# Performance work log

Measured on AMD Instinct MI355X. Metric: run time of the kernel, lower is better.

The kernel has to match this reference:

```python
import jax, jax.numpy as jnp
import numpy as np

B = 16384
DIM = 1024
HEADS = 16
LN_EPS = 1e-5


def setup_inputs() -> dict:
    key = jax.random.key(0)
    ks = jax.random.split(key, 8)
    d = DIM
    s = 0.02
    return {
        "x_u": jax.random.normal(ks[0], (B, d), dtype=jnp.float32),
        "x_m": jax.random.normal(ks[1], (B, d), dtype=jnp.float32),
        # MHA m2u (path 1): packed in_proj [3d, d] like torch, out_proj [d, d]
        "w_qkv1": (jax.random.normal(ks[2], (3 * d, d), dtype=jnp.float32) * s),
        "b_qkv1": jnp.zeros((3 * d,), dtype=jnp.float32),
        "w_o1": (jax.random.normal(ks[3], (d, d), dtype=jnp.float32) * s),
        "b_o1": jnp.zeros((d,), dtype=jnp.float32),
        # MHA u2m (path 2)
        "w_qkv2": (jax.random.normal(ks[4], (3 * d, d), dtype=jnp.float32) * s),
        "b_qkv2": jnp.zeros((3 * d,), dtype=jnp.float32),
        "w_o2": (jax.random.normal(ks[5], (d, d), dtype=jnp.float32) * s),
        "b_o2": jnp.zeros((d,), dtype=jnp.float32),
        # proj head: LayerNorm(2d) + Linear(2d -> d) + GELU (dropout = eval identity)
        "ln_g": jnp.ones((2 * d,), dtype=jnp.float32),
        "ln_b": jnp.zeros((2 * d,), dtype=jnp.float32),
        "w_proj": (jax.random.normal(ks[6], (d, 2 * d), dtype=jnp.float32) * s),
        "b_proj": jnp.zeros((d,), dtype=jnp.float32),
        "heads": HEADS,
    }


def _mha_single_token(xq, xkv, w_qkv, b_qkv, w_o, b_o, heads):
    # seq_len = 1 cross-attention: softmax over a single key is exactly 1.
    d = xq.shape[-1]
    dh = d // heads
    wq, wk, wv = jnp.split(w_qkv, 3, axis=0)
    bq, bk, bv = jnp.split(b_qkv, 3)
    q = (xq @ wq.T + bq).reshape(-1, heads, dh)   # [B, H, dh]
    k = (xkv @ wk.T + bk).reshape(-1, heads, dh)
    v = (xkv @ wv.T + bv).reshape(-1, heads, dh)
    scores = jnp.sum(q * k, axis=-1) / jnp.sqrt(jnp.asarray(dh, q.dtype))  # [B, H]
    attn = jax.nn.softmax(scores[..., None], axis=-1)  # singleton key axis -> ones
    out = (attn * v).reshape(-1, d)                    # [B, d]
    return out @ w_o.T + b_o


def reference(x_u, x_m, w_qkv1, b_qkv1, w_o1, b_o1,
              w_qkv2, b_qkv2, w_o2, b_o2,
              ln_g, ln_b, w_proj, b_proj, heads):
    # Path 1: Q = x_m, K/V = x_u ; Path 2: Q = x_u, K/V = x_m
    z1 = _mha_single_token(x_m, x_u, w_qkv1, b_qkv1, w_o1, b_o1, heads)
    z2 = _mha_single_token(x_u, x_m, w_qkv2, b_qkv2, w_o2, b_o2, heads)
    z = jnp.concatenate([z1, z2], axis=-1)  # [B, 2d]
    mu = jnp.mean(z, axis=-1, keepdims=True)
    var = jnp.mean(jnp.square(z - mu), axis=-1, keepdims=True)
    zn = (z - mu) * jax.lax.rsqrt(var + LN_EPS) * ln_g + ln_b
    h = zn @ w_proj.T + b_proj               # [B, d]
    return jax.nn.gelu(h, approximate=False)  # torch nn.GELU default = exact erf
```

## Files before the change

### kernel.cpp

```cpp
#include <hip/hip_runtime.h>
#include <cstdint>


#define DIM 1024
#define BROWS 16384

typedef __bf16 bf16x8 __attribute__((ext_vector_type(8)));
typedef float f32x4 __attribute__((ext_vector_type(4)));

__device__ __forceinline__ ushort f2bf(float f) {
    uint32_t u = __builtin_bit_cast(uint32_t, f);
    u = (u + 0x7fffu + ((u >> 16) & 1u)) >> 16;
    return (ushort)u;
}

__device__ __forceinline__ void async_copy16(const void* gsrc, void* ldst) {
    __builtin_amdgcn_global_load_lds(
        (__attribute__((address_space(1))) void*)((uintptr_t)gsrc),
        (__attribute__((address_space(3))) void*)((uint32_t)(uintptr_t)ldst),
        16, 0, 0);
}

__global__ __launch_bounds__(256) void prep_kernel(
        const float* __restrict__ x_u, const float* __restrict__ x_m,
        const float* __restrict__ wqkv1, const float* __restrict__ bqkv1,
        const float* __restrict__ wo1, const float* __restrict__ bo1,
        const float* __restrict__ wqkv2, const float* __restrict__ bqkv2,
        const float* __restrict__ wo2, const float* __restrict__ bo2,
        const float* __restrict__ lng, const float* __restrict__ lnb,
        const float* __restrict__ wproj, const float* __restrict__ bproj,
        ushort* __restrict__ x_bf, ushort* __restrict__ wo12,
        ushort* __restrict__ wvT12, ushort* __restrict__ Wp,
        float* __restrict__ b12, float* __restrict__ Svec, float* __restrict__ Cvec,
        float* __restrict__ sums) {
    const int b = blockIdx.x, t = threadIdx.x;
    __shared__ float red[4][4];
    __shared__ float tls[32][33];

    if (b < 8192) {
        const int n4 = (BROWS * DIM) / 4;
        int i = b * 256 + t;
        const int stride = 8192 * 256;
        const float4* xu4 = (const float4*)x_u;
        const float4* xm4 = (const float4*)x_m;
        ushort4* o4 = (ushort4*)x_bf;
#pragma unroll
        for (int it = 0; it < 4; it++, i += stride) {
            float4 v = (i < n4) ? xu4[i] : xm4[i - n4];
            ushort4 o;
            o.x = f2bf(v.x); o.y = f2bf(v.y); o.z = f2bf(v.z); o.w = f2bf(v.w);
            o4[i] = o;
        }
    } else if (b < 9216) {
        int j = b - 8192;
        float s1 = 0.f, s2 = 0.f, sS = 0.f, sC = 0.f;
        for (int c = t; c < DIM; c += 256) {
            s1 += wo1[j * DIM + c] * bqkv1[2 * DIM + c];
            s2 += wo2[j * DIM + c] * bqkv2[2 * DIM + c];
        }
        for (int c = t; c < 2 * DIM; c += 256) {
            float w = wproj[j * 2 * DIM + c];
            sS += w * lng[c];
            sC += w * lnb[c];
        }
        for (int o = 32; o; o >>= 1) {
            s1 += __shfl_down(s1, o, 64);
            s2 += __shfl_down(s2, o, 64);
            sS += __shfl_down(sS, o, 64);
            sC += __shfl_down(sC, o, 64);
        }
        int wid = t >> 6;
        if ((t & 63) == 0) { red[wid][0] = s1; red[wid][1] = s2; red[wid][2] = sS; red[wid][3] = sC; }
        __syncthreads();
        if (t == 0) {
            s1 = red[0][0] + red[1][0] + red[2][0] + red[3][0];
            s2 = red[0][1] + red[1][1] + red[2][1] + red[3][1];
            sS = red[0][2] + red[1][2] + red[2][2] + red[3][2];
            sC = red[0][3] + red[1][3] + red[2][3] + red[3][3];
            b12[j]       = s1 + bo1[j];
            b12[DIM + j] = s2 + bo2[j];
            Svec[j] = sS;
            Cvec[j] = sC + bproj[j];
        }
    } else if (b < 12288) {
        const int NWO = (DIM * DIM) / 4;
        const int NWP = (DIM * 2 * DIM) / 4;
        const int total = 2 * NWO + NWP;
        int i = (b - 9216) * 256 + t;
        const int stride = 3072 * 256;
        for (; i < total; i += stride) {
            if (i < 2 * NWO) {
                float4 v = (i < NWO) ? ((const float4*)wo1)[i] : ((const float4*)wo2)[i - NWO];
                ushort4 o;
                o.x = f2bf(v.x); o.y = f2bf(v.y); o.z = f2bf(v.z); o.w = f2bf(v.w);
                ((ushort4*)wo12)[i] = o;
            } else {
                int j = i - 2 * NWO;
                float4 v = ((const float4*)wproj)[j];
                int c = (j * 4) & (2 * DIM - 1);
                v.x *= lng[c]; v.y *= lng[c + 1]; v.z *= lng[c + 2]; v.w *= lng[c + 3];
                ushort4 o;
                o.x = f2bf(v.x); o.y = f2bf(v.y); o.z = f2bf(v.z); o.w = f2bf(v.w);
                ((ushort4*)Wp)[j] = o;
            }
        }
    } else if (b < 14336) {
        int tile = b - 12288;
        int z = tile >> 10;
        int t2 = tile & 1023;
        int mt = t2 >> 5, kt = t2 & 31;
        const float* src = z ? wqkv2 : wqkv1;
        int tr = t >> 3;
        int tc4 = (t & 7) * 4;
        const float* p = src + (long)(2 * DIM + mt * 32 + tr) * DIM + kt * 32 + tc4;
        float4 v = *(const float4*)p;
        tls[tr][tc4 + 0] = v.x; tls[tr][tc4 + 1] = v.y;
        tls[tr][tc4 + 2] = v.z; tls[tr][tc4 + 3] = v.w;
        __syncthreads();
        ushort4 o;
        o.x = f2bf(tls[tc4 + 0][tr]);
        o.y = f2bf(tls[tc4 + 1][tr]);
        o.z = f2bf(tls[tc4 + 2][tr]);
        o.w = f2bf(tls[tc4 + 3][tr]);
        *(ushort4*)(wvT12 + (long)z * DIM * DIM + (long)(kt * 32 + tr) * DIM + mt * 32 + tc4) = o;
    } else {
        int i = (b - 14336) * 256 + t;
        ((float4*)sums)[i] = float4{0.f, 0.f, 0.f, 0.f};
    }
}

__global__ __launch_bounds__(256, 2) void gemm_w(
        const ushort* __restrict__ Ag, const ushort* __restrict__ Wg,
        ushort* __restrict__ Cg, int K, int lda, int ldw, int ldc,
        long sAz, long sWz, long sCz) {
    constexpr int BM = 64, BN = 64, BK = 32;
    constexpr int MT = BM / 32;
    constexpr int NT = BN / 32;
    __shared__ __align__(16) ushort As[BM * BK];
    __shared__ __align__(16) ushort Bs[BN * BK];
    const int tid = threadIdx.x;
    const int wid = tid >> 6;
    const int lane = tid & 63;
    const int quad = lane >> 4;
    const int l16 = lane & 15;
    const int waveM = wid >> 1, waveN = wid & 1;
    const int zb = blockIdx.z;

    const ushort* A = Ag + zb * sAz + (long)blockIdx.x * BM * lda;
    const ushort* W = Wg + zb * sWz + (long)blockIdx.y * BN * ldw;

    f32x4 acc[MT][NT] = {};
    constexpr int nA = (BM * BK) / (256 * 8);
    constexpr int nB = (BN * BK) / (256 * 8);
    const int swz = (l16 >> 1) & 3;
    const int rdA = quad ^ swz;
    for (int k0 = 0; k0 < K; k0 += BK) {
#pragma unroll
        for (int c = 0; c < nA; c++) {
            int idx = c * 256 + tid;
            int r = idx >> 2;
            int q = (idx & 3) ^ ((r >> 1) & 3);
            async_copy16(A + (long)r * lda + k0 + q * 8, (char*)As + (c * 256 + wid * 64) * 16);
        }
#pragma unroll
        for (int c = 0; c < nB; c++) {
            int idx = c * 256 + tid;
            int r = idx >> 2;
            int q = (idx & 3) ^ ((r >> 1) & 3);
            async_copy16(W + (long)r * ldw + k0 + q * 8, (char*)Bs + (c * 256 + wid * 64) * 16);
        }
        asm volatile("s_waitcnt vmcnt(0)" ::: "memory");
        __syncthreads();

        bf16x8 af[MT], bfg[NT];
#pragma unroll
        for (int im = 0; im < MT; im++)
            af[im] = *(const bf16x8*)(As + (waveM * (BM / 2) + im * 16 + l16) * BK + rdA * 8);
#pragma unroll
        for (int in = 0; in < NT; in++)
            bfg[in] = *(const bf16x8*)(Bs + (waveN * (BN / 2) + in * 16 + l16) * BK + rdA * 8);
#pragma unroll
        for (int im = 0; im < MT; im++)
#pragma unroll
            for (int in = 0; in < NT; in++)
                acc[im][in] = __builtin_amdgcn_mfma_f32_16x16x32_bf16(
                    af[im], bfg[in], acc[im][in], 0, 0, 0);
        __syncthreads();
    }

    const int gRow0 = blockIdx.x * BM + waveM * (BM / 2) + quad * 4;
    const int gCol0 = blockIdx.y * BN + waveN * (BN / 2) + l16;
    ushort* C = Cg + zb * sCz;
#pragma unroll
    for (int im = 0; im < MT; im++)
#pragma unroll
        for (int in = 0; in < NT; in++) {
            int col = gCol0 + in * 16;
#pragma unroll
            for (int r = 0; r < 4; r++) {
                int row = gRow0 + im * 16 + r;
                C[(long)row * ldc + col] = f2bf(acc[im][in][r]);
            }
        }
}

template <int MODE>
__global__ __launch_bounds__(256, 2) void gemm_bt2(
        const ushort* __restrict__ Ag, const ushort* __restrict__ Wg,
        void* __restrict__ Cg, int K, int lda, int ldw, int ldc,
        long sAz, long sWz, long sCz,
        const float* __restrict__ bias,
        const float* __restrict__ Svec, const float* __restrict__ Cvec,
        float* __restrict__ sumbuf, float* __restrict__ sqbuf) {
    __shared__ __align__(16) ushort As[3 * 8192];
    __shared__ __align__(16) ushort Bs[3 * 4096];
    const int tid = threadIdx.x;
    const int wid = tid >> 6;
    const int lane = tid & 63;
    const int quad = lane >> 4;
    const int l16 = lane & 15;
    const int waveM = wid >> 1;
    const int waveN = wid & 1;
    const int zb = blockIdx.z;
    const int rd = quad ^ ((l16 >> 1) & 3);

    const ushort* A = Ag + zb * sAz + (long)blockIdx.x * 256 * lda;
    const ushort* W = Wg + zb * sWz + (long)blockIdx.y * 128 * ldw;
    const int NTK = K >> 5;

    f32x4 acc[8][4] = {};

#pragma unroll
    for (int u = 0; u < 2; ++u) {
        const int k0 = u << 5;
        char* sa = (char*)As + u * 16384;
        char* sb = (char*)Bs + u * 8192;
#pragma unroll
        for (int rnd = 0; rnd < 4; ++rnd) {
            int idx = rnd * 256 + tid;
            int r = idx >> 2;
            int q = (idx & 3) ^ ((r >> 1) & 3);
            async_copy16(A + (long)r * lda + k0 + q * 8, sa + (rnd * 256 + wid * 64) * 16);
        }
#pragma unroll
        for (int rnd = 0; rnd < 2; ++rnd) {
            int idx = rnd * 256 + tid;
            int r = idx >> 2;
            int q = (idx & 3) ^ ((r >> 1) & 3);
            async_copy16(W + (long)r * ldw + k0 + q * 8, sb + (rnd * 256 + wid * 64) * 16);
        }
    }
    asm volatile("s_waitcnt vmcnt(6)" ::: "memory");
    __builtin_amdgcn_s_barrier();
    asm volatile("" ::: "memory");

    int cs = 0, ss = 2;
    for (int t = 0; t < NTK; ++t) {
        const ushort* as = As + cs * 8192;
        const ushort* bs = Bs + cs * 4096;

        bf16x8 af[8], bfg[4];
#pragma unroll
        for (int j = 0; j < 4; ++j)
            bfg[j] = *(const bf16x8*)(bs + (waveN * 64 + j * 16 + l16) * 32 + rd * 8);
#pragma unroll
        for (int i = 0; i < 8; ++i)
            af[i] = *(const bf16x8*)(as + (waveM * 128 + i * 16 + l16) * 32 + rd * 8);

        const int u = t + 2;
        if (u < NTK) {
            const int k0u = u << 5;
            char* sa = (char*)As + ss * 16384;
            char* sb = (char*)Bs + ss * 8192;
#pragma unroll
            for (int rnd = 0; rnd < 4; ++rnd) {
                int idx = rnd * 256 + tid;
                int r = idx >> 2;
                int q = (idx & 3) ^ ((r >> 1) & 3);
                async_copy16(A + (long)r * lda + k0u + q * 8, sa + (rnd * 256 + wid * 64) * 16);
            }
#pragma unroll
            for (int rnd = 0; rnd < 2; ++rnd) {
                int idx = rnd * 256 + tid;
                int r = idx >> 2;
                int q = (idx & 3) ^ ((r >> 1) & 3);
                async_copy16(W + (long)r * ldw + k0u + q * 8, sb + (rnd * 256 + wid * 64) * 16);
            }
        }

        __builtin_amdgcn_s_setprio(1);
#pragma unroll
        for (int i = 0; i < 8; ++i)
#pragma unroll
            for (int j = 0; j < 4; ++j)
                acc[i][j] = __builtin_amdgcn_mfma_f32_16x16x32_bf16(
                    af[i], bfg[j], acc[i][j], 0, 0, 0);
        __builtin_amdgcn_s_setprio(0);

        if (t < NTK - 1) {
            if (t < NTK - 2) asm volatile("s_waitcnt vmcnt(6)" ::: "memory");
            else             asm volatile("s_waitcnt vmcnt(0)" ::: "memory");
            __builtin_amdgcn_s_barrier();
            asm volatile("" ::: "memory");
        }
        cs = (cs == 2) ? 0 : cs + 1;
        ss = (ss == 2) ? 0 : ss + 1;
    }

    const int gRow0 = blockIdx.x * 256 + waveM * 128 + quad * 4;
    const int gCol0 = blockIdx.y * 128 + waveN * 64 + l16;
    if constexpr (MODE == 1) {
        ushort* C = (ushort*)Cg + zb * sCz;
#pragma unroll
        for (int im = 0; im < 8; ++im) {
            float sr[4] = {0.f, 0.f, 0.f, 0.f};
            float qr[4] = {0.f, 0.f, 0.f, 0.f};
#pragma unroll
            for (int in = 0; in < 4; ++in) {
                int col = gCol0 + in * 16;
                float badd = bias[zb * DIM + col];
#pragma unroll
                for (int r = 0; r < 4; ++r) {
                    int row = gRow0 + im * 16 + r;
                    float val = acc[im][in][r] + badd;
                    C[(long)row * ldc + col] = f2bf(val);
                    sr[r] += val;
                    qr[r] += val * val;
                }
            }
#pragma unroll
            for (int r = 0; r < 4; ++r) {
                float s = sr[r], q = qr[r];
#pragma unroll
                for (int o = 1; o < 16; o <<= 1) {
                    s += __shfl_xor(s, o, 64);
                    q += __shfl_xor(q, o, 64);
                }
                if (l16 == 0) {
                    int row = gRow0 + im * 16 + r;
                    atomicAdd(&sumbuf[row], s);
                    atomicAdd(&sqbuf[row], q);
                }
            }
        }
    } else {
        float* O = (float*)Cg;
#pragma unroll
        for (int im = 0; im < 8; ++im) {
#pragma unroll
            for (int r = 0; r < 4; ++r) {
                int row = gRow0 + im * 16 + r;
                float sv = sumbuf[row], qv = sqbuf[row];
                float m = sv * (1.f / 2048.f);
                float var = qv * (1.f / 2048.f) - m * m;
                float rstd = rsqrtf(var + 1e-5f);
#pragma unroll
                for (int in = 0; in < 4; ++in) {
                    int col = gCol0 + in * 16;
                    float h = rstd * (acc[im][in][r] - m * Svec[col]) + Cvec[col];
                    O[(long)row * ldc + col] = 0.5f * h * (1.0f + erff(h * 0.7071067811865475f));
                }
            }
        }
    }
}


extern "C" void kernel_launch(void* const* d_in, const int* in_sizes, int n_in,
                              void* d_out, int out_size, void* d_ws, size_t ws_size,
                              hipStream_t stream) {
    (void)in_sizes; (void)n_in; (void)out_size; (void)ws_size;
    const float* x_u   = (const float*)d_in[0];
    const float* x_m   = (const float*)d_in[1];
    const float* wqkv1 = (const float*)d_in[2];
    const float* bqkv1 = (const float*)d_in[3];
    const float* wo1   = (const float*)d_in[4];
    const float* bo1   = (const float*)d_in[5];
    const float* wqkv2 = (const float*)d_in[6];
    const float* bqkv2 = (const float*)d_in[7];
    const float* wo2   = (const float*)d_in[8];
    const float* bo2   = (const float*)d_in[9];
    const float* lng   = (const float*)d_in[10];
    const float* lnb   = (const float*)d_in[11];
    const float* wproj = (const float*)d_in[12];
    const float* bproj = (const float*)d_in[13];

    char* ws = (char*)d_ws;
    ushort* x_bf  = (ushort*)(ws + 0);
    ushort* wo12  = (ushort*)(ws + 67108864);
    ushort* wvT12 = (ushort*)(ws + 71303168);
    ushort* W12   = (ushort*)(ws + 75497472);
    ushort* Wp    = (ushort*)(ws + 79691776);
    ushort* zbuf  = (ushort*)(ws + 83886080);
    float*  b12   = (float*)(ws + 150994944);
    float*  Svec  = (float*)(ws + 151003136);
    float*  Cvec  = (float*)(ws + 151007232);
    float*  sumbuf= (float*)(ws + 151011328);
    float*  sqbuf = (float*)(ws + 151076864);

    prep_kernel<<<14368, 256, 0, stream>>>(
        x_u, x_m, wqkv1, bqkv1, wo1, bo1, wqkv2, bqkv2, wo2, bo2,
        lng, lnb, wproj, bproj,
        x_bf, wo12, wvT12, Wp, b12, Svec, Cvec, sumbuf);

    gemm_w<<<dim3(16, 16, 2), 256, 0, stream>>>(
        wo12, wvT12, W12, DIM, DIM, DIM, DIM,
        (long)DIM * DIM, (long)DIM * DIM, (long)DIM * DIM);

    gemm_bt2<1><<<dim3(64, 8, 2), 256, 0, stream>>>(
        x_bf, W12, zbuf, DIM, DIM, DIM, 2 * DIM,
        (long)BROWS * DIM, (long)DIM * DIM, (long)DIM,
        b12, nullptr, nullptr, sumbuf, sqbuf);

    gemm_bt2<2><<<dim3(64, 8, 1), 256, 0, stream>>>(
        zbuf, Wp, d_out, 2 * DIM, 2 * DIM, 2 * DIM, DIM,
        0, 0, 0,
        nullptr, Svec, Cvec, sumbuf, sqbuf);
}
```

Baseline: 402.9 us.

## Widen GEMM tiles to 256x256 with BK=64, 512 threads, double buffering

The two main bf16 GEMMs now use 512-thread blocks with 256x256 output tiles and a 64-wide K step. The old 256x128 tiles used a 32-wide K step with triple buffering. Shared-memory staging switches to an 8-way XOR swizzle with two sub-k MFMA passes per stage and a plain double buffer that waits for vmcnt(0) every iteration. The larger tile is meant to raise arithmetic intensity and halve the number of barriers per K. The cost is 128KB of LDS per block, which likely limits occupancy to one block per CU, and less prefetch depth, since each wait drains all loads.

```diff
diff --git a/kernel.cpp b/kernel.cpp
--- a/kernel.cpp
+++ b/kernel.cpp
@@ -205,110 +205,89 @@
 }
 
 template <int MODE>
-__global__ __launch_bounds__(256, 2) void gemm_bt2(
+__global__ __launch_bounds__(512, 2) void gemm_bk64(
         const ushort* __restrict__ Ag, const ushort* __restrict__ Wg,
         void* __restrict__ Cg, int K, int lda, int ldw, int ldc,
         long sAz, long sWz, long sCz,
         const float* __restrict__ bias,
         const float* __restrict__ Svec, const float* __restrict__ Cvec,
         float* __restrict__ sumbuf, float* __restrict__ sqbuf) {
-    __shared__ __align__(16) ushort As[3 * 8192];
-    __shared__ __align__(16) ushort Bs[3 * 4096];
+    __shared__ __align__(16) ushort As[2 * 16384];
+    __shared__ __align__(16) ushort Bs[2 * 16384];
     const int tid = threadIdx.x;
     const int wid = tid >> 6;
     const int lane = tid & 63;
     const int quad = lane >> 4;
     const int l16 = lane & 15;
-    const int waveM = wid >> 1;
-    const int waveN = wid & 1;
+    const int waveM = wid >> 2;
+    const int waveN = wid & 3;
     const int zb = blockIdx.z;
-    const int rd = quad ^ ((l16 >> 1) & 3);
 
     const ushort* A = Ag + zb * sAz + (long)blockIdx.x * 256 * lda;
-    const ushort* W = Wg + zb * sWz + (long)blockIdx.y * 128 * ldw;
-    const int NTK = K >> 5;
+    const ushort* W = Wg + zb * sWz + (long)blockIdx.y * 256 * ldw;
+    const int NTK = K >> 6;
 
     f32x4 acc[8][4] = {};
 
-#pragma unroll
-    for (int u = 0; u < 2; ++u) {
-        const int k0 = u << 5;
-        char* sa = (char*)As + u * 16384;
-        char* sb = (char*)Bs + u * 8192;
+    auto stage = [&](int u, int s) {
+        const int k0 = u << 6;
+        char* sa = (char*)As + s * 32768;
+        char* sb = (char*)Bs + s * 32768;
 #pragma unroll
         for (int rnd = 0; rnd < 4; ++rnd) {
-            int idx = rnd * 256 + tid;
-            int r = idx >> 2;
-            int q = (idx & 3) ^ ((r >> 1) & 3);
-            async_copy16(A + (long)r * lda + k0 + q * 8, sa + (rnd * 256 + wid * 64) * 16);
-        }
-#pragma unroll
-        for (int rnd = 0; rnd < 2; ++rnd) {
-            int idx = rnd * 256 + tid;
-            int r = idx >> 2;
-            int q = (idx & 3) ^ ((r >> 1) & 3);
-            async_copy16(W + (long)r * ldw + k0 + q * 8, sb + (rnd * 256 + wid * 64) * 16);
-        }
-    }
-    asm volatile("s_waitcnt vmcnt(6)" ::: "memory");
+            int idx = rnd * 512 + tid;
+            int r = idx >> 3;
+            int q = (idx & 7) ^ (r & 7);
+            async_copy16(A + (long)r * lda + k0 + q * 8, sa + (rnd * 512 + wid * 64) * 16);
+        }
+#pragma unroll
+        for (int rnd = 0; rnd < 4; ++rnd) {
+            int idx = rnd * 512 + tid;
+            int r = idx >> 3;
+            int q = (idx & 7) ^ (r & 7);
+            async_copy16(W + (long)r * ldw + k0 + q * 8, sb + (rnd * 512 + wid * 64) * 16);
+        }
+    };
+
+    stage(0, 0);
+    asm volatile("s_waitcnt vmcnt(0)" ::: "memory");
     __builtin_amdgcn_s_barrier();
     asm volatile("" ::: "memory");
 
-    int cs = 0, ss = 2;
     for (int t = 0; t < NTK; ++t) {
-        const ushort* as = As + cs * 8192;
-        const ushort* bs = Bs + cs * 4096;
-
-        bf16x8 af[8], bfg[4];
-#pragma unroll
-        for (int j = 0; j < 4; ++j)
-            bfg[j] = *(const bf16x8*)(bs + (waveN * 64 + j * 16 + l16) * 32 + rd * 8);
-#pragma unroll
-        for (int i = 0; i < 8; ++i)
-            af[i] = *(const bf16x8*)(as + (waveM * 128 + i * 16 + l16) * 32 + rd * 8);
-
-        const int u = t + 2;
-        if (u < NTK) {
-            const int k0u = u << 5;
-            char* sa = (char*)As + ss * 16384;
-            char* sb = (char*)Bs + ss * 8192;
-#pragma unroll
-            for (int rnd = 0; rnd < 4; ++rnd) {
-                int idx = rnd * 256 + tid;
-                int r = idx >> 2;
-                int q = (idx & 3) ^ ((r >> 1) & 3);
-                async_copy16(A + (long)r * lda + k0u + q * 8, sa + (rnd * 256 + wid * 64) * 16);
-            }
-#pragma unroll
-            for (int rnd = 0; rnd < 2; ++rnd) {
-                int idx = rnd * 256 + tid;
-                int r = idx >> 2;
-                int q = (idx & 3) ^ ((r >> 1) & 3);
-                async_copy16(W + (long)r * ldw + k0u + q * 8, sb + (rnd * 256 + wid * 64) * 16);
-            }
-        }
-
-        __builtin_amdgcn_s_setprio(1);
-#pragma unroll
-        for (int i = 0; i < 8; ++i)
+        const ushort* as = As + (t & 1) * 16384;
+        const ushort* bs = Bs + (t & 1) * 16384;
+        if (t + 1 < NTK) stage(t + 1, (t + 1) & 1);
+
+#pragma unroll
+        for (int ks = 0; ks < 2; ++ks) {
+            bf16x8 af[8], bfg[4];
+            const int rq = ((ks * 4 + quad) ^ (l16 & 7)) * 8;
 #pragma unroll
             for (int j = 0; j < 4; ++j)
-                acc[i][j] = __builtin_amdgcn_mfma_f32_16x16x32_bf16(
-                    af[i], bfg[j], acc[i][j], 0, 0, 0);
-        __builtin_amdgcn_s_setprio(0);
-
-        if (t < NTK - 1) {
-            if (t < NTK - 2) asm volatile("s_waitcnt vmcnt(6)" ::: "memory");
-            else             asm volatile("s_waitcnt vmcnt(0)" ::: "memory");
+                bfg[j] = *(const bf16x8*)(bs + (waveN * 64 + j * 16 + l16) * 64 + rq);
+#pragma unroll
+            for (int i = 0; i < 8; ++i)
+                af[i] = *(const bf16x8*)(as + (waveM * 128 + i * 16 + l16) * 64 + rq);
+            __builtin_amdgcn_s_setprio(1);
+#pragma unroll
+            for (int i = 0; i < 8; ++i)
+#pragma unroll
+                for (int j = 0; j < 4; ++j)
+                    acc[i][j] = __builtin_amdgcn_mfma_f32_16x16x32_bf16(
+                        af[i], bfg[j], acc[i][j], 0, 0, 0);
+            __builtin_amdgcn_s_setprio(0);
+        }
+
+        if (t + 1 < NTK) {
+            asm volatile("s_waitcnt vmcnt(0)" ::: "memory");
             __builtin_amdgcn_s_barrier();
             asm volatile("" ::: "memory");
         }
-        cs = (cs == 2) ? 0 : cs + 1;
-        ss = (ss == 2) ? 0 : ss + 1;
     }
 
     const int gRow0 = blockIdx.x * 256 + waveM * 128 + quad * 4;
-    const int gCol0 = blockIdx.y * 128 + waveN * 64 + l16;
+    const int gCol0 = blockIdx.y * 256 + waveN * 64 + l16;
     if constexpr (MODE == 1) {
         ushort* C = (ushort*)Cg + zb * sCz;
 #pragma unroll
@@ -407,12 +386,12 @@
         wo12, wvT12, W12, DIM, DIM, DIM, DIM,
         (long)DIM * DIM, (long)DIM * DIM, (long)DIM * DIM);
 
-    gemm_bt2<1><<<dim3(64, 8, 2), 256, 0, stream>>>(
+    gemm_bk64<1><<<dim3(64, 4, 2), 512, 0, stream>>>(
         x_bf, W12, zbuf, DIM, DIM, DIM, 2 * DIM,
         (long)BROWS * DIM, (long)DIM * DIM, (long)DIM,
         b12, nullptr, nullptr, sumbuf, sqbuf);
 
-    gemm_bt2<2><<<dim3(64, 8, 1), 256, 0, stream>>>(
+    gemm_bk64<2><<<dim3(64, 4, 1), 512, 0, stream>>>(
         zbuf, Wp, d_out, 2 * DIM, 2 * DIM, 2 * DIM, DIM,
         0, 0, 0,
         nullptr, Svec, Cvec, sumbuf, sqbuf);
```

Result: faster. 384.9 us (-4.5%).
